# Kernel tuning notes

Hardware: AMD Instinct MI355X
Metric: run time of the kernel (lower is better)

Reference implementation:

```python
import jax, jax.numpy as jnp
import numpy as np

N_NODES = 131072
N_EDGES = 262144
N_GRAPHS = 4096
EMB = 300
N_LAYERS = 5
N_TASKS = 12
N_EXPERTS = 8
GATE_DIM = 300
NUM_ATOM_TYPE = 120
NUM_CHIRALITY = 3
NUM_BOND_TYPE = 6
NUM_BOND_DIR = 3


def setup_inputs() -> dict:
    key = jax.random.key(0)
    ks = jax.random.split(key, 24)
    x = jnp.stack([
        jax.random.randint(ks[0], (N_NODES,), 0, NUM_ATOM_TYPE),
        jax.random.randint(ks[1], (N_NODES,), 0, NUM_CHIRALITY),
    ], axis=1)
    edge_index = jax.random.randint(ks[2], (2, N_EDGES), 0, N_NODES)
    edge_attr = jnp.stack([
        jax.random.randint(ks[3], (N_EDGES,), 0, NUM_BOND_TYPE),
        jax.random.randint(ks[4], (N_EDGES,), 0, NUM_BOND_DIR),
    ], axis=1)
    batch = jnp.sort(jax.random.randint(ks[5], (N_NODES,), 0, N_GRAPHS))

    s = 0.05
    atom_emb1 = jax.random.normal(ks[6], (NUM_ATOM_TYPE, EMB)) * s
    atom_emb2 = jax.random.normal(ks[7], (NUM_CHIRALITY, EMB)) * s
    edge_emb1 = jax.random.normal(ks[8], (N_LAYERS, NUM_BOND_TYPE, EMB)) * s
    edge_emb2 = jax.random.normal(ks[9], (N_LAYERS, NUM_BOND_DIR, EMB)) * s
    mlp_w1 = jax.random.normal(ks[10], (N_LAYERS, EMB, 2 * EMB)) * s
    mlp_b1 = jnp.zeros((N_LAYERS, 2 * EMB))
    mlp_w2 = jax.random.normal(ks[11], (N_LAYERS, 2 * EMB, EMB)) * s
    mlp_b2 = jnp.zeros((N_LAYERS, EMB))
    bn_gamma = jnp.ones((N_LAYERS, EMB))
    bn_beta = jnp.zeros((N_LAYERS, EMB))
    gate_w1 = jax.random.normal(ks[12], (EMB, GATE_DIM)) * s
    gate_b1 = jnp.zeros((GATE_DIM,))
    gate_bn_g = jnp.ones((GATE_DIM,))
    gate_bn_b = jnp.zeros((GATE_DIM,))
    gate_w2 = jax.random.normal(ks[13], (GATE_DIM, GATE_DIM)) * s
    gate_b2 = jnp.zeros((GATE_DIM,))
    cluster = jax.random.normal(ks[14], (N_EXPERTS, GATE_DIM)) * s
    experts_w = jax.random.normal(ks[15], (EMB, N_TASKS * N_EXPERTS)) * s
    experts_b = jnp.zeros((N_TASKS * N_EXPERTS,))
    return dict(x=x, edge_index=edge_index, edge_attr=edge_attr, batch=batch,
                atom_emb1=atom_emb1, atom_emb2=atom_emb2,
                edge_emb1=edge_emb1, edge_emb2=edge_emb2,
                mlp_w1=mlp_w1, mlp_b1=mlp_b1, mlp_w2=mlp_w2, mlp_b2=mlp_b2,
                bn_gamma=bn_gamma, bn_beta=bn_beta,
                gate_w1=gate_w1, gate_b1=gate_b1,
                gate_bn_g=gate_bn_g, gate_bn_b=gate_bn_b,
                gate_w2=gate_w2, gate_b2=gate_b2,
                cluster=cluster, experts_w=experts_w, experts_b=experts_b)


def _batchnorm(h, g, b, eps=1e-5):
    mu = h.mean(axis=0)
    var = h.var(axis=0)
    return g * (h - mu) * jax.lax.rsqrt(var + eps) + b


def _forward(x, edge_index, edge_attr, batch,
             atom_emb1, atom_emb2, edge_emb1, edge_emb2,
             mlp_w1, mlp_b1, mlp_w2, mlp_b2, bn_gamma, bn_beta,
             gate_w1, gate_b1, gate_bn_g, gate_bn_b, gate_w2, gate_b2,
             cluster, experts_w, experts_b):
    n = x.shape[0]
    src, dst = edge_index[0], edge_index[1]
    ea0, ea1 = edge_attr[:, 0], edge_attr[:, 1]
    # node input embedding
    h = atom_emb1[x[:, 0]] + atom_emb2[x[:, 1]]  # [N, EMB]
    n_layers = mlp_w1.shape[0]
    for l in range(n_layers):
        ee = edge_emb1[l][ea0] + edge_emb2[l][ea1]  # [E, EMB]
        # self loops: attr = (bond_type=4, dir=0) for every node
        self_ee = edge_emb1[l][4] + edge_emb2[l][0]  # [EMB]
        agg = jax.ops.segment_sum(h[src] + ee, dst, num_segments=n)
        agg = agg + h + self_ee  # self-loop messages
        hid = jax.nn.relu(agg @ mlp_w1[l] + mlp_b1[l])
        h = hid @ mlp_w2[l] + mlp_b2[l]
        h = _batchnorm(h, bn_gamma[l], bn_beta[l])
        if l < n_layers - 1:
            h = jax.nn.relu(h)
    # graph pooling (JK='last')
    sums = jax.ops.segment_sum(h, batch, num_segments=N_GRAPHS)  # [B, EMB]
    counts = jax.ops.segment_sum(jnp.ones((n, 1), h.dtype), batch, num_segments=N_GRAPHS)
    gnn_out = sums / jnp.maximum(counts, 1.0)  # mean pool
    gate_input = sums  # global_add_pool
    # experts head: sum(gnn_out[:, :, None] * W, dim=1) + b == gnn_out @ W + b
    n_experts = cluster.shape[0]
    clf_logit = (gnn_out @ experts_w + experts_b).reshape(N_GRAPHS, -1, n_experts)
    # gate network
    zh = _batchnorm(gate_input @ gate_w1 + gate_b1, gate_bn_g, gate_bn_b)
    z = jax.nn.relu(zh) @ gate_w2 + gate_b2  # [B, GATE_DIM]
    # q: temperature-scaled softmax over cosine similarity to cluster centroids
    zn = z / jnp.maximum(jnp.linalg.norm(z, axis=1, keepdims=True), 1e-6)
    cn = cluster / jnp.maximum(jnp.linalg.norm(cluster, axis=1, keepdims=True), 1e-6)
    q = jax.nn.softmax(10.0 * (zn @ cn.T), axis=-1)  # T = 10
    return clf_logit, z, q


def reference(x, edge_index, edge_attr, batch,
              atom_emb1, atom_emb2, edge_emb1, edge_emb2,
              mlp_w1, mlp_b1, mlp_w2, mlp_b2, bn_gamma, bn_beta,
              gate_w1, gate_b1, gate_bn_g, gate_bn_b, gate_w2, gate_b2,
              cluster, experts_w, experts_b):
    return _forward(x, edge_index, edge_attr, batch,
                    atom_emb1, atom_emb2, edge_emb1, edge_emb2,
                    mlp_w1, mlp_b1, mlp_w2, mlp_b2, bn_gamma, bn_beta,
                    gate_w1, gate_b1, gate_bn_g, gate_bn_b, gate_w2, gate_b2,
                    cluster, experts_w, experts_b)
```

## Files before the change

kernel.cpp:

```cpp
#include <hip/hip_runtime.h>
#include <hip/hip_bf16.h>

typedef unsigned short u16;
typedef unsigned int u32;

#define NN 131072
#define NE 262144
#define NG 4096
#define EMB 300
#define HID 600
#define NL 5
#define NTNE 96
#define NEXP 8

#define W1T_ROWS 640
#define W1T_K    328
#define W2T_ROWS 384
#define W2T_K    648

typedef __attribute__((ext_vector_type(8)))  short  s16x8;
typedef __attribute__((ext_vector_type(8)))  __bf16 b16x8;
typedef __attribute__((ext_vector_type(16))) float  f32x16;

static __device__ __forceinline__ float u2f(u16 u) {
    union { u32 i; float f; } w; w.i = ((u32)u) << 16; return w.f;
}
static __device__ __forceinline__ u16 f2u(float f) {
    union { float f; u32 i; } w; w.f = f;
    return (u16)((w.i + 0x7fffu + ((w.i >> 16) & 1u)) >> 16);
}

static __device__ __forceinline__ f32x16 mfma_3216(s16x8 a, s16x8 b, f32x16 c) {
    return __builtin_amdgcn_mfma_f32_32x32x16_bf16(
        __builtin_bit_cast(b16x8, a), __builtin_bit_cast(b16x8, b), c, 0, 0, 0);
}

__global__ void k_zero(float* __restrict__ p, int n) {
    int i = blockIdx.x * 256 + threadIdx.x;
    if (i < n) p[i] = 0.f;
}
__global__ void k_zero_int(int* __restrict__ p, int n) {
    int i = blockIdx.x * 256 + threadIdx.x;
    if (i < n) p[i] = 0;
}

__global__ void k_embed(const int* __restrict__ x, const float* __restrict__ ae1,
                        const float* __restrict__ ae2, u16* __restrict__ h) {
    int i = blockIdx.x;
    int a0 = x[2 * i], a1 = x[2 * i + 1];
    for (int f = threadIdx.x; f < EMB; f += blockDim.x)
        h[(size_t)i * EMB + f] = f2u(ae1[a0 * EMB + f] + ae2[a1 * EMB + f]);
}

__global__ void k_hist(const int* __restrict__ ei, int* __restrict__ deg) {
    int e = blockIdx.x * 256 + threadIdx.x;
    if (e < NE) atomicAdd(&deg[ei[NE + e]], 1);
}

__global__ __launch_bounds__(1024) void k_scan(const int* __restrict__ deg,
                                               int* __restrict__ rowstart) {
    __shared__ int lds[1024];
    int tid = threadIdx.x;
    int base = tid * 128;
    int s = 0;
    for (int j = 0; j < 128; ++j) s += deg[base + j];
    lds[tid] = s;
    __syncthreads();
    for (int off = 1; off < 1024; off <<= 1) {
        int v = (tid >= off) ? lds[tid - off] : 0;
        __syncthreads();
        lds[tid] += v;
        __syncthreads();
    }
    int run = (tid == 0) ? 0 : lds[tid - 1];
    for (int j = 0; j < 128; ++j) {
        rowstart[base + j] = run;
        run += deg[base + j];
    }
    if (tid == 1023) rowstart[NN] = run;
}

__global__ void k_fill(const int* __restrict__ ei, const int* __restrict__ ea,
                       int* __restrict__ deg, const int* __restrict__ rowstart,
                       u32* __restrict__ payload) {
    int e = blockIdx.x * 256 + threadIdx.x;
    if (e >= NE) return;
    int src = ei[e], dst = ei[NE + e];
    int c = ea[2 * e] * 3 + ea[2 * e + 1];
    int old = atomicSub(&deg[dst], 1);
    int pos = rowstart[dst] + old - 1;
    payload[pos] = (u32)src | ((u32)c << 17);
}

__global__ void k_prep_w1(const float* __restrict__ w1, u16* __restrict__ w1t) {
    int n = blockIdx.x;
    int l = blockIdx.y;
    size_t dst = ((size_t)l * W1T_ROWS + n) * W1T_K;
    for (int k = threadIdx.x; k < W1T_K; k += blockDim.x) {
        u16 v = 0;
        if (n < HID && k < EMB) v = f2u(w1[(size_t)l * EMB * HID + (size_t)k * HID + n]);
        w1t[dst + k] = v;
    }
}
__global__ void k_prep_w2(const float* __restrict__ w2, u16* __restrict__ w2t) {
    int n = blockIdx.x;
    int l = blockIdx.y;
    size_t dst = ((size_t)l * W2T_ROWS + n) * W2T_K;
    for (int k = threadIdx.x; k < W2T_K; k += blockDim.x) {
        u16 v = 0;
        if (n < EMB && k < HID) v = f2u(w2[(size_t)l * HID * EMB + (size_t)k * EMB + n]);
        w2t[dst + k] = v;
    }
}

template <bool APPLY_BN>
__global__ __launch_bounds__(512) void k_layer1(const u16* __restrict__ h,
                                                const u32* __restrict__ payload,
                                                const int* __restrict__ rowstart,
                                                const float* __restrict__ e1,
                                                const float* __restrict__ e2,
                                                const float* __restrict__ stats,
                                                const float* __restrict__ bg,
                                                const float* __restrict__ bb,
                                                float invM,
                                                const u16* __restrict__ w1t,
                                                const float* __restrict__ b1,
                                                u16* __restrict__ hid) {
    __shared__ __align__(16) u16 ee_lds[18 * 300];
    __shared__ __align__(16) u16 scale_s[300];
    __shared__ __align__(16) u16 shift_s[300];
    __shared__ __align__(16) u16 A_s[64 * 328];
    int tid = threadIdx.x;
    int lane = tid & 63, wid = tid >> 6;
    int wr = wid >> 2, wc = wid & 3;
    int l31 = lane & 31, lhi = lane >> 5;
    size_t rowBase = (size_t)blockIdx.x * 64;

    for (int idx = tid; idx < 18 * 300; idx += 512) {
        int c = idx / 300, f = idx - c * 300;
        ee_lds[idx] = f2u(e1[(c / 3) * 300 + f] + e2[(c % 3) * 300 + f]);
    }
    if (APPLY_BN) {
        if (tid < 300) {
            float mu = stats[tid] * invM;
            float var = stats[EMB + tid] * invM - mu * mu;
            float sc = bg[tid] * rsqrtf(var + 1e-5f);
            scale_s[tid] = f2u(sc);
            shift_s[tid] = f2u(bb[tid] - mu * sc);
        }
    }
    for (int idx = tid; idx < 64 * 28; idx += 512)
        A_s[(idx / 28) * 328 + 300 + (idx % 28)] = 0;
    __syncthreads();

    for (int task = tid; task < 64 * 75; task += 512) {
        int r = task / 75, fc = task - r * 75;
        int i = (int)rowBase + r;
        int f0 = fc * 4;
        int beg = rowstart[i], end = rowstart[i + 1];
        float sc0 = 1.f, sc1 = 1.f, sc2 = 1.f, sc3 = 1.f;
        float sh0 = 0.f, sh1 = 0.f, sh2 = 0.f, sh3 = 0.f;
        if (APPLY_BN) {
            ushort4 scv = *(const ushort4*)&scale_s[f0];
            ushort4 shv = *(const ushort4*)&shift_s[f0];
            sc0 = u2f(scv.x); sc1 = u2f(scv.y); sc2 = u2f(scv.z); sc3 = u2f(scv.w);
            sh0 = u2f(shv.x); sh1 = u2f(shv.y); sh2 = u2f(shv.z); sh3 = u2f(shv.w);
        }
        ushort4 hv = *(const ushort4*)&h[(size_t)i * EMB + f0];
        ushort4 ev = *(const ushort4*)&ee_lds[12 * 300 + f0];
        float a0 = u2f(hv.x), a1 = u2f(hv.y), a2 = u2f(hv.z), a3 = u2f(hv.w);
        if (APPLY_BN) {
            a0 = fmaxf(a0 * sc0 + sh0, 0.f);
            a1 = fmaxf(a1 * sc1 + sh1, 0.f);
            a2 = fmaxf(a2 * sc2 + sh2, 0.f);
            a3 = fmaxf(a3 * sc3 + sh3, 0.f);
        }
        float v0 = a0 + u2f(ev.x), v1 = a1 + u2f(ev.y);
        float v2 = a2 + u2f(ev.z), v3 = a3 + u2f(ev.w);
        for (int e = beg; e < end; ++e) {
            u32 p = payload[e];
            int src = p & 0x1FFFF;
            ushort4 ec = *(const ushort4*)&ee_lds[(int)(p >> 17) * 300 + f0];
            ushort4 sv = *(const ushort4*)&h[(size_t)src * EMB + f0];
            float g0 = u2f(sv.x), g1 = u2f(sv.y), g2 = u2f(sv.z), g3 = u2f(sv.w);
            if (APPLY_BN) {
                g0 = fmaxf(g0 * sc0 + sh0, 0.f);
                g1 = fmaxf(g1 * sc1 + sh1, 0.f);
                g2 = fmaxf(g2 * sc2 + sh2, 0.f);
                g3 = fmaxf(g3 * sc3 + sh3, 0.f);
            }
            v0 += g0 + u2f(ec.x);
            v1 += g1 + u2f(ec.y);
            v2 += g2 + u2f(ec.z);
            v3 += g3 + u2f(ec.w);
        }
        short4 o;
        o.x = (short)f2u(v0); o.y = (short)f2u(v1);
        o.z = (short)f2u(v2); o.w = (short)f2u(v3);
        *(short4*)&A_s[r * 328 + f0] = o;
    }
    __syncthreads();

    s16x8 afr[20];
    int abase = (wr * 32 + l31) * 328 + lhi * 8;
#pragma unroll
    for (int s = 0; s < 20; ++s) afr[s] = *(const s16x8*)&A_s[abase + s * 16];

    for (int c5 = 0; c5 < 5; ++c5) {
        int col = c5 * 128 + wc * 32 + l31;
        const u16* bp = w1t + (size_t)col * W1T_K + lhi * 8;
        f32x16 acc = {};
#pragma unroll
        for (int s = 0; s < 20; ++s)
            acc = mfma_3216(afr[s], *(const s16x8*)&bp[s * 16], acc);
        if (col < HID) {
            float bias = b1[col];
#pragma unroll
            for (int r = 0; r < 16; ++r) {
                int row = (r & 3) + 8 * (r >> 2) + 4 * lhi;
                hid[(rowBase + wr * 32 + row) * HID + col] =
                    f2u(fmaxf(acc[r] + bias, 0.f));
            }
        }
    }
}

__global__ __launch_bounds__(256) void k_gemm2(const u16* __restrict__ hid,
                                               const u16* __restrict__ w2t,
                                               const float* __restrict__ b2,
                                               u16* __restrict__ hout) {
    __shared__ __align__(16) u16 A_s[64 * 72];
    __shared__ __align__(16) u16 B_s[128 * 72];
    int tid = threadIdx.x;
    int lane = tid & 63, wid = tid >> 6;
    int wr = wid >> 1, wc = wid & 1;
    int l31 = lane & 31, lhi = lane >> 5;
    size_t rowBase = (size_t)blockIdx.x * 64;
    int cc = blockIdx.y * 128;

    f32x16 acc0 = {}, acc1 = {};
    int aoff = (wr * 32 + l31) * 72 + lhi * 8;
    int boff0 = (wc * 64 + l31) * 72 + lhi * 8;
    int boff1 = boff0 + 32 * 72;

    for (int sl = 0; sl < 10; ++sl) {
        int k0 = sl * 64;
        for (int idx = tid; idx < 512; idx += 256) {
            int m = idx >> 3, kv = idx & 7;
            int k = k0 + kv * 8;
            s16x8 v = {};
            if (k < HID) v = *(const s16x8*)&hid[(rowBase + m) * HID + k];
            *(s16x8*)&A_s[m * 72 + kv * 8] = v;
        }
        for (int idx = tid; idx < 1024; idx += 256) {
            int n = idx >> 3, kv = idx & 7;
            *(s16x8*)&B_s[n * 72 + kv * 8] =
                *(const s16x8*)&w2t[(size_t)(cc + n) * W2T_K + k0 + kv * 8];
        }
        __syncthreads();

        int smax = (sl < 9) ? 4 : 2;
        for (int s = 0; s < smax; ++s) {
            s16x8 a  = *(const s16x8*)&A_s[aoff + s * 16];
            s16x8 ba = *(const s16x8*)&B_s[boff0 + s * 16];
            s16x8 bb = *(const s16x8*)&B_s[boff1 + s * 16];
            acc0 = mfma_3216(a, ba, acc0);
            acc1 = mfma_3216(a, bb, acc1);
        }
        __syncthreads();
    }

    int colA = cc + wc * 64 + l31;
    int colB = colA + 32;
    if (colA < EMB) {
        float bias = b2[colA];
#pragma unroll
        for (int r = 0; r < 16; ++r) {
            int row = (r & 3) + 8 * (r >> 2) + 4 * lhi;
            hout[(rowBase + wr * 32 + row) * EMB + colA] = f2u(acc0[r] + bias);
        }
    }
    if (colB < EMB) {
        float bias = b2[colB];
#pragma unroll
        for (int r = 0; r < 16; ++r) {
            int row = (r & 3) + 8 * (r >> 2) + 4 * lhi;
            hout[(rowBase + wr * 32 + row) * EMB + colB] = f2u(acc1[r] + bias);
        }
    }
}

__global__ void k_bn_stats_h(const u16* __restrict__ X, float* __restrict__ stats) {
    int t = threadIdx.x;
    int half = t / 160;
    int pr = t - half * 160;
    if (pr >= 150) return;
    float s0 = 0.f, s1 = 0.f, q0 = 0.f, q1 = 0.f;
    for (int r = blockIdx.x * 2 + half; r < NN; r += 512) {
        u32 v = *(const u32*)&X[(size_t)r * EMB + pr * 2];
        float a = u2f((u16)(v & 0xffff));
        float b = u2f((u16)(v >> 16));
        s0 += a; s1 += b; q0 += a * a; q1 += b * b;
    }
    atomicAdd(&stats[2 * pr], s0);
    atomicAdd(&stats[2 * pr + 1], s1);
    atomicAdd(&stats[EMB + 2 * pr], q0);
    atomicAdd(&stats[EMB + 2 * pr + 1], q1);
}

template <bool RELU>
__global__ void k_bn_apply_h(u16* __restrict__ X, const float* __restrict__ stats,
                             const float* __restrict__ g, const float* __restrict__ b, float invM) {
    int r = blockIdx.x;
    for (int f = threadIdx.x; f < EMB; f += blockDim.x) {
        float mu = stats[f] * invM;
        float var = stats[EMB + f] * invM - mu * mu;
        float v = (u2f(X[(size_t)r * EMB + f]) - mu) * rsqrtf(var + 1e-5f) * g[f] + b[f];
        if (RELU) v = fmaxf(v, 0.f);
        X[(size_t)r * EMB + f] = f2u(v);
    }
}

__global__ void k_bn_stats_f(const float* __restrict__ X, int M, float* __restrict__ stats) {
    int f = threadIdx.x;
    if (f >= EMB) return;
    float s = 0.f, s2 = 0.f;
    for (int r = blockIdx.x; r < M; r += gridDim.x) {
        float v = X[(size_t)r * EMB + f];
        s += v;
        s2 += v * v;
    }
    atomicAdd(&stats[f], s);
    atomicAdd(&stats[EMB + f], s2);
}

template <bool RELU>
__global__ void k_bn_apply_f(float* __restrict__ X, const float* __restrict__ stats,
                             const float* __restrict__ g, const float* __restrict__ b, float invM) {
    int r = blockIdx.x;
    for (int f = threadIdx.x; f < EMB; f += blockDim.x) {
// ... 124 lines not shown
        float v = z[(size_t)gi * EMB + f];
        s += v * v;
    }
    for (int o = 32; o; o >>= 1) s += __shfl_xor(s, o);
    float zn = fmaxf(sqrtf(s), 1e-6f);
    float sc[NEXP];
#pragma unroll
    for (int e = 0; e < NEXP; ++e) {
        float d = 0.f;
        for (int f = l; f < EMB; f += 64) d += z[(size_t)gi * EMB + f] * cluster[e * EMB + f];
        for (int o = 32; o; o >>= 1) d += __shfl_xor(d, o);
        sc[e] = 10.f * d / (zn * fmaxf(cnorm[e], 1e-6f));
    }
    float mx = sc[0];
#pragma unroll
    for (int e = 1; e < NEXP; ++e) mx = fmaxf(mx, sc[e]);
    float se = 0.f;
#pragma unroll
    for (int e = 0; e < NEXP; ++e) {
        sc[e] = expf(sc[e] - mx);
        se += sc[e];
    }
    if (l < NEXP) qout[(size_t)gi * NEXP + l] = sc[l] / se;
}

extern "C" void kernel_launch(void* const* d_in, const int* in_sizes, int n_in,
                              void* d_out, int out_size, void* d_ws, size_t ws_size,
                              hipStream_t stream) {
    const int* x       = (const int*)d_in[0];
    const int* ei      = (const int*)d_in[1];
    const int* ea      = (const int*)d_in[2];
    const int* batch   = (const int*)d_in[3];
    const float* ae1   = (const float*)d_in[4];
    const float* ae2   = (const float*)d_in[5];
    const float* ee1   = (const float*)d_in[6];
    const float* ee2   = (const float*)d_in[7];
    const float* w1    = (const float*)d_in[8];
    const float* b1    = (const float*)d_in[9];
    const float* w2    = (const float*)d_in[10];
    const float* b2    = (const float*)d_in[11];
    const float* bng   = (const float*)d_in[12];
    const float* bnb   = (const float*)d_in[13];
    const float* gw1   = (const float*)d_in[14];
    const float* gb1   = (const float*)d_in[15];
    const float* gbng  = (const float*)d_in[16];
    const float* gbnb  = (const float*)d_in[17];
    const float* gw2   = (const float*)d_in[18];
    const float* gb2   = (const float*)d_in[19];
    const float* clus  = (const float*)d_in[20];
    const float* ew    = (const float*)d_in[21];
    const float* eb    = (const float*)d_in[22];

    char* wp = (char*)d_ws;
    u16* hbuf = (u16*)wp;                 wp += (size_t)NN * EMB * sizeof(u16);
    u16* hid = (u16*)wp;                  wp += (size_t)NN * HID * sizeof(u16);
    float* stats = (float*)wp;            wp += 2 * EMB * sizeof(float);
    u16* w1t = (u16*)wp;                  wp += (size_t)NL * W1T_ROWS * W1T_K * sizeof(u16);
    u16* w2t = (u16*)wp;                  wp += (size_t)NL * W2T_ROWS * W2T_K * sizeof(u16);
    int* deg = (int*)wp;                  wp += (size_t)NN * sizeof(int);
    int* rowstart = (int*)wp;             wp += (size_t)(NN + 4) * sizeof(int);
    u32* payload = (u32*)wp;              wp += (size_t)NE * sizeof(u32);

    float* sums   = (float*)hid;
    float* counts = sums + (size_t)NG * EMB;
    float* zh     = counts + NG;
    float* zb     = zh + (size_t)NG * EMB;
    float* cnorm  = zb + (size_t)NG * EMB;

    float* out     = (float*)d_out;
    float* out_clf = out;
    float* out_z   = out + (size_t)NG * NTNE;
    float* out_q   = out_z + (size_t)NG * EMB;

    k_zero_int<<<NN / 256, 256, 0, stream>>>(deg, NN);
    k_hist<<<NE / 256, 256, 0, stream>>>(ei, deg);
    k_scan<<<1, 1024, 0, stream>>>(deg, rowstart);
    k_fill<<<NE / 256, 256, 0, stream>>>(ei, ea, deg, rowstart, payload);

    k_prep_w1<<<dim3(W1T_ROWS, NL), 64, 0, stream>>>(w1, w1t);
    k_prep_w2<<<dim3(W2T_ROWS, NL), 64, 0, stream>>>(w2, w2t);
    k_embed<<<NN, 320, 0, stream>>>(x, ae1, ae2, hbuf);

    for (int l = 0; l < NL; ++l) {
        const float* e1 = ee1 + (size_t)l * 6 * EMB;
        const float* e2 = ee2 + (size_t)l * 3 * EMB;
        if (l == 0)
            k_layer1<false><<<NN / 64, 512, 0, stream>>>(
                hbuf, payload, rowstart, e1, e2, nullptr, nullptr, nullptr, 0.f,
                w1t + (size_t)l * W1T_ROWS * W1T_K, b1 + (size_t)l * HID, hid);
        else
            k_layer1<true><<<NN / 64, 512, 0, stream>>>(
                hbuf, payload, rowstart, e1, e2, stats,
                bng + (size_t)(l - 1) * EMB, bnb + (size_t)(l - 1) * EMB, 1.f / NN,
                w1t + (size_t)l * W1T_ROWS * W1T_K, b1 + (size_t)l * HID, hid);
        k_gemm2<<<dim3(NN / 64, 3), 256, 0, stream>>>(hid, w2t + (size_t)l * W2T_ROWS * W2T_K,
                                                      b2 + (size_t)l * EMB, hbuf);
        k_zero<<<3, 256, 0, stream>>>(stats, 2 * EMB);
        k_bn_stats_h<<<256, 320, 0, stream>>>(hbuf, stats);
    }

    k_bn_apply_h<false><<<NN, 320, 0, stream>>>(hbuf, stats, bng + (size_t)(NL - 1) * EMB,
                                                bnb + (size_t)(NL - 1) * EMB, 1.f / NN);

    k_pool<<<NG, 320, 0, stream>>>(hbuf, batch, sums, counts);
    k_clf<<<NG, 128, 0, stream>>>(sums, counts, ew, eb, out_clf);

    k_gemm<false><<<dim3(5, NG / 64), 256, 0, stream>>>(sums, gw1, gb1, zh, NG, EMB, EMB);
    k_zero<<<3, 256, 0, stream>>>(stats, 2 * EMB);
    k_bn_stats_f<<<256, 320, 0, stream>>>(zh, NG, stats);
    k_bn_apply_f<true><<<NG, 320, 0, stream>>>(zh, stats, gbng, gbnb, 1.f / NG);
    k_gemm<false><<<dim3(5, NG / 64), 256, 0, stream>>>(zh, gw2, gb2, zb, NG, EMB, EMB);

    k_cnorm<<<1, 64, 0, stream>>>(clus, cnorm);
    k_zout<<<NG, 320, 0, stream>>>(zb, out_z);
    k_q<<<NG, 64, 0, stream>>>(zb, clus, cnorm, out_q);
}
```

Before: 3.047 ms.

## Fuse second MLP GEMM into layer kernel, keep hidden tile in LDS

The second GEMM is now computed inside the aggregation plus first-GEMM kernel. Each 128-column chunk of the hidden activation is staged in LDS and multiplied straight into three accumulators per wave, so the NN×600 bf16 hidden tensor is no longer written to and re-read from global memory. Because a block now reads neighbour rows of h while other blocks write the layer output, h is ping-ponged between two buffers. The edge gather loop is also unrolled by two to issue more loads per iteration. In exchange, w2 is read directly from global memory by every block, two extra block barriers are added per chunk, and LDS use grows by about 17 KB per block.

```diff
diff --git a/kernel.cpp b/kernel.cpp
--- a/kernel.cpp
+++ b/kernel.cpp
@@ -114,22 +114,25 @@
 }
 
 template <bool APPLY_BN>
-__global__ __launch_bounds__(512) void k_layer1(const u16* __restrict__ h,
-                                                const u32* __restrict__ payload,
-                                                const int* __restrict__ rowstart,
-                                                const float* __restrict__ e1,
-                                                const float* __restrict__ e2,
-                                                const float* __restrict__ stats,
-                                                const float* __restrict__ bg,
-                                                const float* __restrict__ bb,
-                                                float invM,
-                                                const u16* __restrict__ w1t,
-                                                const float* __restrict__ b1,
-                                                u16* __restrict__ hid) {
+__global__ __launch_bounds__(512, 4) void k_layer_fused(const u16* __restrict__ h,
+                                                        const u32* __restrict__ payload,
+                                                        const int* __restrict__ rowstart,
+                                                        const float* __restrict__ e1,
+                                                        const float* __restrict__ e2,
+                                                        const float* __restrict__ stats,
+                                                        const float* __restrict__ bg,
+                                                        const float* __restrict__ bb,
+                                                        float invM,
+                                                        const u16* __restrict__ w1t,
+                                                        const float* __restrict__ b1,
+                                                        const u16* __restrict__ w2t,
+                                                        const float* __restrict__ b2,
+                                                        u16* __restrict__ hout) {
     __shared__ __align__(16) u16 ee_lds[18 * 300];
     __shared__ __align__(16) u16 scale_s[300];
     __shared__ __align__(16) u16 shift_s[300];
     __shared__ __align__(16) u16 A_s[64 * 328];
+    __shared__ __align__(16) u16 H_s[64 * 136];
     int tid = threadIdx.x;
     int lane = tid & 63, wid = tid >> 6;
     int wr = wid >> 2, wc = wid & 3;
@@ -177,7 +180,28 @@
         }
         float v0 = a0 + u2f(ev.x), v1 = a1 + u2f(ev.y);
         float v2 = a2 + u2f(ev.z), v3 = a3 + u2f(ev.w);
-        for (int e = beg; e < end; ++e) {
+        int e = beg;
+        for (; e + 2 <= end; e += 2) {
+            u32 p0 = payload[e], p1 = payload[e + 1];
+            int sA = p0 & 0x1FFFF, sB = p1 & 0x1FFFF;
+            ushort4 svA = *(const ushort4*)&h[(size_t)sA * EMB + f0];
+            ushort4 svB = *(const ushort4*)&h[(size_t)sB * EMB + f0];
+            ushort4 ecA = *(const ushort4*)&ee_lds[(int)(p0 >> 17) * 300 + f0];
+            ushort4 ecB = *(const ushort4*)&ee_lds[(int)(p1 >> 17) * 300 + f0];
+            float gA0 = u2f(svA.x), gA1 = u2f(svA.y), gA2 = u2f(svA.z), gA3 = u2f(svA.w);
+            float gB0 = u2f(svB.x), gB1 = u2f(svB.y), gB2 = u2f(svB.z), gB3 = u2f(svB.w);
+            if (APPLY_BN) {
+                gA0 = fmaxf(gA0 * sc0 + sh0, 0.f); gB0 = fmaxf(gB0 * sc0 + sh0, 0.f);
+                gA1 = fmaxf(gA1 * sc1 + sh1, 0.f); gB1 = fmaxf(gB1 * sc1 + sh1, 0.f);
+                gA2 = fmaxf(gA2 * sc2 + sh2, 0.f); gB2 = fmaxf(gB2 * sc2 + sh2, 0.f);
+                gA3 = fmaxf(gA3 * sc3 + sh3, 0.f); gB3 = fmaxf(gB3 * sc3 + sh3, 0.f);
+            }
+            v0 += gA0 + u2f(ecA.x) + gB0 + u2f(ecB.x);
+            v1 += gA1 + u2f(ecA.y) + gB1 + u2f(ecB.y);
+            v2 += gA2 + u2f(ecA.z) + gB2 + u2f(ecB.z);
+            v3 += gA3 + u2f(ecA.w) + gB3 + u2f(ecB.w);
+        }
+        if (e < end) {
             u32 p = payload[e];
             int src = p & 0x1FFFF;
             ushort4 ec = *(const ushort4*)&ee_lds[(int)(p >> 17) * 300 + f0];
@@ -201,91 +225,72 @@
     }
     __syncthreads();
 
-    s16x8 afr[20];
+    f32x16 acc20 = {}, acc21 = {}, acc22 = {};
     int abase = (wr * 32 + l31) * 328 + lhi * 8;
-#pragma unroll
-    for (int s = 0; s < 20; ++s) afr[s] = *(const s16x8*)&A_s[abase + s * 16];
+    int arow2 = (wr * 32 + l31) * 136 + lhi * 8;
+    int colp = wc * 32 + l31;
 
     for (int c5 = 0; c5 < 5; ++c5) {
-        int col = c5 * 128 + wc * 32 + l31;
-        const u16* bp = w1t + (size_t)col * W1T_K + lhi * 8;
-        f32x16 acc = {};
+        int col1 = c5 * 128 + colp;
+        const u16* bp = w1t + (size_t)col1 * W1T_K + lhi * 8;
+        f32x16 acc1 = {};
 #pragma unroll
         for (int s = 0; s < 20; ++s)
-            acc = mfma_3216(afr[s], *(const s16x8*)&bp[s * 16], acc);
-        if (col < HID) {
-            float bias = b1[col];
+            acc1 = mfma_3216(*(const s16x8*)&A_s[abase + s * 16],
+                             *(const s16x8*)&bp[s * 16], acc1);
+        bool valid = col1 < HID;
+        float bias1 = valid ? b1[col1] : 0.f;
+#pragma unroll
+        for (int r = 0; r < 16; ++r) {
+            int row = (r & 3) + 8 * (r >> 2) + 4 * lhi;
+            float v = valid ? fmaxf(acc1[r] + bias1, 0.f) : 0.f;
+            H_s[(wr * 32 + row) * 136 + colp] = f2u(v);
+        }
+        __syncthreads();
+
+#pragma unroll
+        for (int kk = 0; kk < 8; ++kk) {
+            s16x8 a = *(const s16x8*)&H_s[arow2 + kk * 16];
+            int gk = c5 * 128 + kk * 16 + lhi * 8;
+            const u16* wb = w2t + gk;
+            acc20 = mfma_3216(a, *(const s16x8*)&wb[(size_t)(wc * 96 + l31) * W2T_K], acc20);
+            acc21 = mfma_3216(a, *(const s16x8*)&wb[(size_t)(wc * 96 + 32 + l31) * W2T_K], acc21);
+            acc22 = mfma_3216(a, *(const s16x8*)&wb[(size_t)(wc * 96 + 64 + l31) * W2T_K], acc22);
+        }
+        __syncthreads();
+    }
+
+    {
+        int col = wc * 96 + l31;
+        if (col < EMB) {
+            float bias = b2[col];
 #pragma unroll
             for (int r = 0; r < 16; ++r) {
                 int row = (r & 3) + 8 * (r >> 2) + 4 * lhi;
-                hid[(rowBase + wr * 32 + row) * HID + col] =
-                    f2u(fmaxf(acc[r] + bias, 0.f));
+                hout[(rowBase + wr * 32 + row) * EMB + col] = f2u(acc20[r] + bias);
             }
         }
     }
-}
-
-__global__ __launch_bounds__(256) void k_gemm2(const u16* __restrict__ hid,
-                                               const u16* __restrict__ w2t,
-                                               const float* __restrict__ b2,
-                                               u16* __restrict__ hout) {
-    __shared__ __align__(16) u16 A_s[64 * 72];
-    __shared__ __align__(16) u16 B_s[128 * 72];
-    int tid = threadIdx.x;
-    int lane = tid & 63, wid = tid >> 6;
-    int wr = wid >> 1, wc = wid & 1;
-    int l31 = lane & 31, lhi = lane >> 5;
-    size_t rowBase = (size_t)blockIdx.x * 64;
-    int cc = blockIdx.y * 128;
-
-    f32x16 acc0 = {}, acc1 = {};
-    int aoff = (wr * 32 + l31) * 72 + lhi * 8;
-    int boff0 = (wc * 64 + l31) * 72 + lhi * 8;
-    int boff1 = boff0 + 32 * 72;
-
-    for (int sl = 0; sl < 10; ++sl) {
-        int k0 = sl * 64;
-        for (int idx = tid; idx < 512; idx += 256) {
-            int m = idx >> 3, kv = idx & 7;
-            int k = k0 + kv * 8;
-            s16x8 v = {};
-            if (k < HID) v = *(const s16x8*)&hid[(rowBase + m) * HID + k];
-            *(s16x8*)&A_s[m * 72 + kv * 8] = v;
-        }
-        for (int idx = tid; idx < 1024; idx += 256) {
-            int n = idx >> 3, kv = idx & 7;
-            *(s16x8*)&B_s[n * 72 + kv * 8] =
-                *(const s16x8*)&w2t[(size_t)(cc + n) * W2T_K + k0 + kv * 8];
-        }
-        __syncthreads();
-
-        int smax = (sl < 9) ? 4 : 2;
-        for (int s = 0; s < smax; ++s) {
-            s16x8 a  = *(const s16x8*)&A_s[aoff + s * 16];
-            s16x8 ba = *(const s16x8*)&B_s[boff0 + s * 16];
-            s16x8 bb = *(const s16x8*)&B_s[boff1 + s * 16];
-            acc0 = mfma_3216(a, ba, acc0);
-            acc1 = mfma_3216(a, bb, acc1);
-        }
-        __syncthreads();
-    }
-
-    int colA = cc + wc * 64 + l31;
-    int colB = colA + 32;
-    if (colA < EMB) {
-        float bias = b2[colA];
-#pragma unroll
-        for (int r = 0; r < 16; ++r) {
-            int row = (r & 3) + 8 * (r >> 2) + 4 * lhi;
-            hout[(rowBase + wr * 32 + row) * EMB + colA] = f2u(acc0[r] + bias);
-        }
-    }
-    if (colB < EMB) {
-        float bias = b2[colB];
-#pragma unroll
-        for (int r = 0; r < 16; ++r) {
-            int row = (r & 3) + 8 * (r >> 2) + 4 * lhi;
-            hout[(rowBase + wr * 32 + row) * EMB + colB] = f2u(acc1[r] + bias);
+    {
+        int col = wc * 96 + 32 + l31;
+        if (col < EMB) {
+            float bias = b2[col];
+#pragma unroll
+            for (int r = 0; r < 16; ++r) {
+                int row = (r & 3) + 8 * (r >> 2) + 4 * lhi;
+                hout[(rowBase + wr * 32 + row) * EMB + col] = f2u(acc21[r] + bias);
+            }
+        }
+    }
+    {
+        int col = wc * 96 + 64 + l31;
+        if (col < EMB) {
+            float bias = b2[col];
+#pragma unroll
+            for (int r = 0; r < 16; ++r) {
+                int row = (r & 3) + 8 * (r >> 2) + 4 * lhi;
+                hout[(rowBase + wr * 32 + row) * EMB + col] = f2u(acc22[r] + bias);
+            }
         }
     }
 }
@@ -516,8 +521,9 @@
     const float* eb    = (const float*)d_in[22];
 
     char* wp = (char*)d_ws;
-    u16* hbuf = (u16*)wp;                 wp += (size_t)NN * EMB * sizeof(u16);
-    u16* hid = (u16*)wp;                  wp += (size_t)NN * HID * sizeof(u16);
+    u16* hA = (u16*)wp;                   wp += (size_t)NN * EMB * sizeof(u16);
+    u16* hB = (u16*)wp;                   wp += (size_t)NN * EMB * sizeof(u16);
+    float* scratch = (float*)wp;          wp += ((size_t)NG * EMB * 3 + NG + NEXP + 64) * sizeof(float);
     float* stats = (float*)wp;            wp += 2 * EMB * sizeof(float);
     u16* w1t = (u16*)wp;                  wp += (size_t)NL * W1T_ROWS * W1T_K * sizeof(u16);
     u16* w2t = (u16*)wp;                  wp += (size_t)NL * W2T_ROWS * W2T_K * sizeof(u16);
@@ -525,7 +531,7 @@
     int* rowstart = (int*)wp;             wp += (size_t)(NN + 4) * sizeof(int);
     u32* payload = (u32*)wp;              wp += (size_t)NE * sizeof(u32);
 
-    float* sums   = (float*)hid;
+    float* sums   = scratch;
     float* counts = sums + (size_t)NG * EMB;
     float* zh     = counts + NG;
     float* zb     = zh + (size_t)NG * EMB;
@@ -543,30 +549,33 @@
 
     k_prep_w1<<<dim3(W1T_ROWS, NL), 64, 0, stream>>>(w1, w1t);
     k_prep_w2<<<dim3(W2T_ROWS, NL), 64, 0, stream>>>(w2, w2t);
-    k_embed<<<NN, 320, 0, stream>>>(x, ae1, ae2, hbuf);
-
+    k_embed<<<NN, 320, 0, stream>>>(x, ae1, ae2, hA);
+
+    u16* hin = hA;
+    u16* hno = hB;
     for (int l = 0; l < NL; ++l) {
         const float* e1 = ee1 + (size_t)l * 6 * EMB;
         const float* e2 = ee2 + (size_t)l * 3 * EMB;
         if (l == 0)
-            k_layer1<false><<<NN / 64, 512, 0, stream>>>(
-                hbuf, payload, rowstart, e1, e2, nullptr, nullptr, nullptr, 0.f,
-                w1t + (size_t)l * W1T_ROWS * W1T_K, b1 + (size_t)l * HID, hid);
+            k_layer_fused<false><<<NN / 64, 512, 0, stream>>>(
+                hin, payload, rowstart, e1, e2, nullptr, nullptr, nullptr, 0.f,
+                w1t + (size_t)l * W1T_ROWS * W1T_K, b1 + (size_t)l * HID,
+                w2t + (size_t)l * W2T_ROWS * W2T_K, b2 + (size_t)l * EMB, hno);
         else
-            k_layer1<true><<<NN / 64, 512, 0, stream>>>(
-                hbuf, payload, rowstart, e1, e2, stats,
+            k_layer_fused<true><<<NN / 64, 512, 0, stream>>>(
+                hin, payload, rowstart, e1, e2, stats,
                 bng + (size_t)(l - 1) * EMB, bnb + (size_t)(l - 1) * EMB, 1.f / NN,
-                w1t + (size_t)l * W1T_ROWS * W1T_K, b1 + (size_t)l * HID, hid);
-        k_gemm2<<<dim3(NN / 64, 3), 256, 0, stream>>>(hid, w2t + (size_t)l * W2T_ROWS * W2T_K,
-                                                      b2 + (size_t)l * EMB, hbuf);
+                w1t + (size_t)l * W1T_ROWS * W1T_K, b1 + (size_t)l * HID,
+                w2t + (size_t)l * W2T_ROWS * W2T_K, b2 + (size_t)l * EMB, hno);
         k_zero<<<3, 256, 0, stream>>>(stats, 2 * EMB);
-        k_bn_stats_h<<<256, 320, 0, stream>>>(hbuf, stats);
-    }
-
-    k_bn_apply_h<false><<<NN, 320, 0, stream>>>(hbuf, stats, bng + (size_t)(NL - 1) * EMB,
+        k_bn_stats_h<<<256, 320, 0, stream>>>(hno, stats);
+        u16* t = hin; hin = hno; hno = t;
+    }
+
+    k_bn_apply_h<false><<<NN, 320, 0, stream>>>(hin, stats, bng + (size_t)(NL - 1) * EMB,
                                                 bnb + (size_t)(NL - 1) * EMB, 1.f / NN);
 
-    k_pool<<<NG, 320, 0, stream>>>(hbuf, batch, sums, counts);
+    k_pool<<<NG, 320, 0, stream>>>(hin, batch, sums, counts);
     k_clf<<<NG, 128, 0, stream>>>(sums, counts, ew, eb, out_clf);
 
     k_gemm<false><<<dim3(5, NG / 64), 256, 0, stream>>>(sums, gw1, gb1, zh, NG, EMB, EMB);
```

Result: slower. 3.221 ms (+5.7%).

## Precompute edge embeddings and BN params globally; gather two rows per thread

Applied to the files above, without the earlier changes.

Moves the per-block construction of the 18 combined edge-embedding rows and the BN scale/shift into small one-time prep kernels that write bf16 tables to global memory. The aggregation loop then reads those tables through the cache instead of LDS, which cuts per-block setup work and LDS use. Each thread now handles two destination rows at once, interleaving their neighbour gathers to expose more memory-level parallelism. The cost is extra global and cache traffic for the edge-table lookups, higher register pressure, and two small extra launches.

```diff
diff --git a/kernel.cpp b/kernel.cpp
--- a/kernel.cpp
+++ b/kernel.cpp
@@ -17,6 +17,7 @@
 #define W1T_K    328
 #define W2T_ROWS 384
 #define W2T_K    648
+#define EE_S     304
 
 typedef __attribute__((ext_vector_type(8)))  short  s16x8;
 typedef __attribute__((ext_vector_type(8)))  __bf16 b16x8;
@@ -113,22 +114,43 @@
     }
 }
 
+__global__ void k_prep_ee(const float* __restrict__ ee1, const float* __restrict__ ee2,
+                          u16* __restrict__ eeT) {
+    int c = blockIdx.x;
+    int l = blockIdx.y;
+    size_t dst = ((size_t)l * 18 + c) * EE_S;
+    const float* e1 = ee1 + (size_t)l * 6 * EMB + (c / 3) * EMB;
+    const float* e2 = ee2 + (size_t)l * 3 * EMB + (c % 3) * EMB;
+    for (int f = threadIdx.x; f < EE_S; f += blockDim.x)
+        eeT[dst + f] = (f < EMB) ? f2u(e1[f] + e2[f]) : (u16)0;
+}
+
+__global__ void k_prep_bn(const float* __restrict__ stats, const float* __restrict__ bg,
+                          const float* __restrict__ bb, float invM,
+                          u16* __restrict__ scT, u16* __restrict__ shT) {
+    int t = threadIdx.x;
+    if (t >= EE_S) return;
+    if (t < EMB) {
+        float mu = stats[t] * invM;
+        float var = stats[EMB + t] * invM - mu * mu;
+        float sc = bg[t] * rsqrtf(var + 1e-5f);
+        scT[t] = f2u(sc);
+        shT[t] = f2u(bb[t] - mu * sc);
+    } else {
+        scT[t] = 0; shT[t] = 0;
+    }
+}
+
 template <bool APPLY_BN>
 __global__ __launch_bounds__(512) void k_layer1(const u16* __restrict__ h,
                                                 const u32* __restrict__ payload,
                                                 const int* __restrict__ rowstart,
-                                                const float* __restrict__ e1,
-                                                const float* __restrict__ e2,
-                                                const float* __restrict__ stats,
-                                                const float* __restrict__ bg,
-                                                const float* __restrict__ bb,
-                                                float invM,
+                                                const u16* __restrict__ eeT,
+                                                const u16* __restrict__ scT,
+                                                const u16* __restrict__ shT,
                                                 const u16* __restrict__ w1t,
                                                 const float* __restrict__ b1,
                                                 u16* __restrict__ hid) {
-    __shared__ __align__(16) u16 ee_lds[18 * 300];
-    __shared__ __align__(16) u16 scale_s[300];
-    __shared__ __align__(16) u16 shift_s[300];
     __shared__ __align__(16) u16 A_s[64 * 328];
     int tid = threadIdx.x;
     int lane = tid & 63, wid = tid >> 6;
@@ -136,52 +158,68 @@
     int l31 = lane & 31, lhi = lane >> 5;
     size_t rowBase = (size_t)blockIdx.x * 64;
 
-    for (int idx = tid; idx < 18 * 300; idx += 512) {
-        int c = idx / 300, f = idx - c * 300;
-        ee_lds[idx] = f2u(e1[(c / 3) * 300 + f] + e2[(c % 3) * 300 + f]);
-    }
-    if (APPLY_BN) {
-        if (tid < 300) {
-            float mu = stats[tid] * invM;
-            float var = stats[EMB + tid] * invM - mu * mu;
-            float sc = bg[tid] * rsqrtf(var + 1e-5f);
-            scale_s[tid] = f2u(sc);
-            shift_s[tid] = f2u(bb[tid] - mu * sc);
-        }
-    }
     for (int idx = tid; idx < 64 * 28; idx += 512)
         A_s[(idx / 28) * 328 + 300 + (idx % 28)] = 0;
     __syncthreads();
 
-    for (int task = tid; task < 64 * 75; task += 512) {
-        int r = task / 75, fc = task - r * 75;
-        int i = (int)rowBase + r;
+    for (int task = tid; task < 32 * 75; task += 512) {
+        int pr = task / 75, fc = task - pr * 75;
         int f0 = fc * 4;
-        int beg = rowstart[i], end = rowstart[i + 1];
+        int iA = (int)rowBase + pr;
+        int iB = iA + 32;
+        int begA = rowstart[iA], endA = rowstart[iA + 1];
+        int begB = rowstart[iB], endB = rowstart[iB + 1];
         float sc0 = 1.f, sc1 = 1.f, sc2 = 1.f, sc3 = 1.f;
         float sh0 = 0.f, sh1 = 0.f, sh2 = 0.f, sh3 = 0.f;
         if (APPLY_BN) {
-            ushort4 scv = *(const ushort4*)&scale_s[f0];
-            ushort4 shv = *(const ushort4*)&shift_s[f0];
+            ushort4 scv = *(const ushort4*)&scT[f0];
+            ushort4 shv = *(const ushort4*)&shT[f0];
             sc0 = u2f(scv.x); sc1 = u2f(scv.y); sc2 = u2f(scv.z); sc3 = u2f(scv.w);
             sh0 = u2f(shv.x); sh1 = u2f(shv.y); sh2 = u2f(shv.z); sh3 = u2f(shv.w);
         }
-        ushort4 hv = *(const ushort4*)&h[(size_t)i * EMB + f0];
-        ushort4 ev = *(const ushort4*)&ee_lds[12 * 300 + f0];
-        float a0 = u2f(hv.x), a1 = u2f(hv.y), a2 = u2f(hv.z), a3 = u2f(hv.w);
+        ushort4 ev = *(const ushort4*)&eeT[12 * EE_S + f0];
+        float e0 = u2f(ev.x), e1v = u2f(ev.y), e2v = u2f(ev.z), e3 = u2f(ev.w);
+
+        ushort4 hvA = *(const ushort4*)&h[(size_t)iA * EMB + f0];
+        ushort4 hvB = *(const ushort4*)&h[(size_t)iB * EMB + f0];
+        float vA0 = u2f(hvA.x), vA1 = u2f(hvA.y), vA2 = u2f(hvA.z), vA3 = u2f(hvA.w);
+        float vB0 = u2f(hvB.x), vB1 = u2f(hvB.y), vB2 = u2f(hvB.z), vB3 = u2f(hvB.w);
         if (APPLY_BN) {
-            a0 = fmaxf(a0 * sc0 + sh0, 0.f);
-            a1 = fmaxf(a1 * sc1 + sh1, 0.f);
-            a2 = fmaxf(a2 * sc2 + sh2, 0.f);
-            a3 = fmaxf(a3 * sc3 + sh3, 0.f);
-        }
-        float v0 = a0 + u2f(ev.x), v1 = a1 + u2f(ev.y);
-        float v2 = a2 + u2f(ev.z), v3 = a3 + u2f(ev.w);
-        for (int e = beg; e < end; ++e) {
-            u32 p = payload[e];
+            vA0 = fmaxf(vA0 * sc0 + sh0, 0.f); vB0 = fmaxf(vB0 * sc0 + sh0, 0.f);
+            vA1 = fmaxf(vA1 * sc1 + sh1, 0.f); vB1 = fmaxf(vB1 * sc1 + sh1, 0.f);
+            vA2 = fmaxf(vA2 * sc2 + sh2, 0.f); vB2 = fmaxf(vB2 * sc2 + sh2, 0.f);
+            vA3 = fmaxf(vA3 * sc3 + sh3, 0.f); vB3 = fmaxf(vB3 * sc3 + sh3, 0.f);
+        }
+        vA0 += e0; vA1 += e1v; vA2 += e2v; vA3 += e3;
+        vB0 += e0; vB1 += e1v; vB2 += e2v; vB3 += e3;
+
+        int eA = begA, eB = begB;
+        while (eA < endA && eB < endB) {
+            u32 pA = payload[eA], pB = payload[eB];
+            int sA = pA & 0x1FFFF, sB = pB & 0x1FFFF;
+            ushort4 svA = *(const ushort4*)&h[(size_t)sA * EMB + f0];
+            ushort4 svB = *(const ushort4*)&h[(size_t)sB * EMB + f0];
+            ushort4 ecA = *(const ushort4*)&eeT[(size_t)(pA >> 17) * EE_S + f0];
+            ushort4 ecB = *(const ushort4*)&eeT[(size_t)(pB >> 17) * EE_S + f0];
+            float gA0 = u2f(svA.x), gA1 = u2f(svA.y), gA2 = u2f(svA.z), gA3 = u2f(svA.w);
+            float gB0 = u2f(svB.x), gB1 = u2f(svB.y), gB2 = u2f(svB.z), gB3 = u2f(svB.w);
+            if (APPLY_BN) {
+                gA0 = fmaxf(gA0 * sc0 + sh0, 0.f); gB0 = fmaxf(gB0 * sc0 + sh0, 0.f);
+                gA1 = fmaxf(gA1 * sc1 + sh1, 0.f); gB1 = fmaxf(gB1 * sc1 + sh1, 0.f);
+                gA2 = fmaxf(gA2 * sc2 + sh2, 0.f); gB2 = fmaxf(gB2 * sc2 + sh2, 0.f);
+                gA3 = fmaxf(gA3 * sc3 + sh3, 0.f); gB3 = fmaxf(gB3 * sc3 + sh3, 0.f);
+            }
+            vA0 += gA0 + u2f(ecA.x); vB0 += gB0 + u2f(ecB.x);
+            vA1 += gA1 + u2f(ecA.y); vB1 += gB1 + u2f(ecB.y);
+            vA2 += gA2 + u2f(ecA.z); vB2 += gB2 + u2f(ecB.z);
+            vA3 += gA3 + u2f(ecA.w); vB3 += gB3 + u2f(ecB.w);
+            ++eA; ++eB;
+        }
+        for (; eA < endA; ++eA) {
+            u32 p = payload[eA];
             int src = p & 0x1FFFF;
-            ushort4 ec = *(const ushort4*)&ee_lds[(int)(p >> 17) * 300 + f0];
             ushort4 sv = *(const ushort4*)&h[(size_t)src * EMB + f0];
+            ushort4 ec = *(const ushort4*)&eeT[(size_t)(p >> 17) * EE_S + f0];
             float g0 = u2f(sv.x), g1 = u2f(sv.y), g2 = u2f(sv.z), g3 = u2f(sv.w);
             if (APPLY_BN) {
                 g0 = fmaxf(g0 * sc0 + sh0, 0.f);
@@ -189,15 +227,35 @@
                 g2 = fmaxf(g2 * sc2 + sh2, 0.f);
                 g3 = fmaxf(g3 * sc3 + sh3, 0.f);
             }
-            v0 += g0 + u2f(ec.x);
-            v1 += g1 + u2f(ec.y);
-            v2 += g2 + u2f(ec.z);
-            v3 += g3 + u2f(ec.w);
-        }
-        short4 o;
-        o.x = (short)f2u(v0); o.y = (short)f2u(v1);
-        o.z = (short)f2u(v2); o.w = (short)f2u(v3);
-        *(short4*)&A_s[r * 328 + f0] = o;
+            vA0 += g0 + u2f(ec.x);
+            vA1 += g1 + u2f(ec.y);
+            vA2 += g2 + u2f(ec.z);
+            vA3 += g3 + u2f(ec.w);
+        }
+        for (; eB < endB; ++eB) {
+            u32 p = payload[eB];
+            int src = p & 0x1FFFF;
+            ushort4 sv = *(const ushort4*)&h[(size_t)src * EMB + f0];
+            ushort4 ec = *(const ushort4*)&eeT[(size_t)(p >> 17) * EE_S + f0];
+            float g0 = u2f(sv.x), g1 = u2f(sv.y), g2 = u2f(sv.z), g3 = u2f(sv.w);
+            if (APPLY_BN) {
+                g0 = fmaxf(g0 * sc0 + sh0, 0.f);
+                g1 = fmaxf(g1 * sc1 + sh1, 0.f);
+                g2 = fmaxf(g2 * sc2 + sh2, 0.f);
+                g3 = fmaxf(g3 * sc3 + sh3, 0.f);
+            }
+            vB0 += g0 + u2f(ec.x);
+            vB1 += g1 + u2f(ec.y);
+            vB2 += g2 + u2f(ec.z);
+            vB3 += g3 + u2f(ec.w);
+        }
+        short4 oA, oB;
+        oA.x = (short)f2u(vA0); oA.y = (short)f2u(vA1);
+        oA.z = (short)f2u(vA2); oA.w = (short)f2u(vA3);
+        oB.x = (short)f2u(vB0); oB.y = (short)f2u(vB1);
+        oB.z = (short)f2u(vB2); oB.w = (short)f2u(vB3);
+        *(short4*)&A_s[pr * 328 + f0] = oA;
+        *(short4*)&A_s[(pr + 32) * 328 + f0] = oB;
     }
     __syncthreads();
 
@@ -521,6 +579,9 @@
     float* stats = (float*)wp;            wp += 2 * EMB * sizeof(float);
     u16* w1t = (u16*)wp;                  wp += (size_t)NL * W1T_ROWS * W1T_K * sizeof(u16);
     u16* w2t = (u16*)wp;                  wp += (size_t)NL * W2T_ROWS * W2T_K * sizeof(u16);
+    u16* eeT = (u16*)wp;                  wp += (size_t)NL * 18 * EE_S * sizeof(u16);
+    u16* scT = (u16*)wp;                  wp += EE_S * sizeof(u16);
+    u16* shT = (u16*)wp;                  wp += EE_S * sizeof(u16);
     int* deg = (int*)wp;                  wp += (size_t)NN * sizeof(int);
     int* rowstart = (int*)wp;             wp += (size_t)(NN + 4) * sizeof(int);
     u32* payload = (u32*)wp;              wp += (size_t)NE * sizeof(u32);
@@ -543,24 +604,26 @@
 
     k_prep_w1<<<dim3(W1T_ROWS, NL), 64, 0, stream>>>(w1, w1t);
     k_prep_w2<<<dim3(W2T_ROWS, NL), 64, 0, stream>>>(w2, w2t);
+    k_prep_ee<<<dim3(18, NL), 128, 0, stream>>>(ee1, ee2, eeT);
     k_embed<<<NN, 320, 0, stream>>>(x, ae1, ae2, hbuf);
 
     for (int l = 0; l < NL; ++l) {
-        const float* e1 = ee1 + (size_t)l * 6 * EMB;
-        const float* e2 = ee2 + (size_t)l * 3 * EMB;
+        const u16* eeL = eeT + (size_t)l * 18 * EE_S;
         if (l == 0)
             k_layer1<false><<<NN / 64, 512, 0, stream>>>(
-                hbuf, payload, rowstart, e1, e2, nullptr, nullptr, nullptr, 0.f,
+                hbuf, payload, rowstart, eeL, nullptr, nullptr,
                 w1t + (size_t)l * W1T_ROWS * W1T_K, b1 + (size_t)l * HID, hid);
         else
             k_layer1<true><<<NN / 64, 512, 0, stream>>>(
-                hbuf, payload, rowstart, e1, e2, stats,
-                bng + (size_t)(l - 1) * EMB, bnb + (size_t)(l - 1) * EMB, 1.f / NN,
+                hbuf, payload, rowstart, eeL, scT, shT,
                 w1t + (size_t)l * W1T_ROWS * W1T_K, b1 + (size_t)l * HID, hid);
         k_gemm2<<<dim3(NN / 64, 3), 256, 0, stream>>>(hid, w2t + (size_t)l * W2T_ROWS * W2T_K,
                                                       b2 + (size_t)l * EMB, hbuf);
         k_zero<<<3, 256, 0, stream>>>(stats, 2 * EMB);
         k_bn_stats_h<<<256, 320, 0, stream>>>(hbuf, stats);
+        if (l < NL - 1)
+            k_prep_bn<<<1, 320, 0, stream>>>(stats, bng + (size_t)l * EMB,
+                                             bnb + (size_t)l * EMB, 1.f / NN, scT, shT);
     }
 
     k_bn_apply_h<false><<<NN, 320, 0, stream>>>(hbuf, stats, bng + (size_t)(NL - 1) * EMB,
```

Result: no change. 3.006 ms, median of 3 (-1.3%).

## Precompute edge embeddings and BN affine once; shrink layer1 blocks to 32 rows

Applied to the files above, without the earlier changes.

Edge-embedding sums and the BatchNorm scale/shift are now computed once by small prep kernels instead of in every layer1 block's shared memory. That lets layer1 use 32-row, 256-thread blocks with much less LDS, which should raise occupancy and hide gather latency. The gemm2 grid is also transposed so the three column tiles of a row block run adjacently, improving L2 reuse of the A rows. In exchange, edge-embedding lookups become global/L1 reads rather than LDS reads, and each W1 tile is reloaded by twice as many blocks.

```diff
diff --git a/kernel.cpp b/kernel.cpp
--- a/kernel.cpp
+++ b/kernel.cpp
@@ -17,6 +17,7 @@
 #define W1T_K    328
 #define W2T_ROWS 384
 #define W2T_K    648
+#define EE_S     304
 
 typedef __attribute__((ext_vector_type(8)))  short  s16x8;
 typedef __attribute__((ext_vector_type(8)))  __bf16 b16x8;
@@ -113,61 +114,68 @@
     }
 }
 
+__global__ void k_prep_ee(const float* __restrict__ ee1, const float* __restrict__ ee2,
+                          u16* __restrict__ eeT) {
+    int c = blockIdx.x;
+    int l = blockIdx.y;
+    size_t dst = ((size_t)l * 18 + c) * EE_S;
+    const float* e1 = ee1 + (size_t)l * 6 * EMB + (c / 3) * EMB;
+    const float* e2 = ee2 + (size_t)l * 3 * EMB + (c % 3) * EMB;
+    for (int f = threadIdx.x; f < EE_S; f += blockDim.x)
+        eeT[dst + f] = (f < EMB) ? f2u(e1[f] + e2[f]) : (u16)0;
+}
+
+__global__ void k_prep_bn(const float* __restrict__ stats, const float* __restrict__ bg,
+                          const float* __restrict__ bb, float invM,
+                          u16* __restrict__ scT, u16* __restrict__ shT) {
+    int t = threadIdx.x;
+    if (t >= EE_S) return;
+    if (t < EMB) {
+        float mu = stats[t] * invM;
+        float var = stats[EMB + t] * invM - mu * mu;
+        float sc = bg[t] * rsqrtf(var + 1e-5f);
+        scT[t] = f2u(sc);
+        shT[t] = f2u(bb[t] - mu * sc);
+    } else {
+        scT[t] = 0; shT[t] = 0;
+    }
+}
+
 template <bool APPLY_BN>
-__global__ __launch_bounds__(512) void k_layer1(const u16* __restrict__ h,
+__global__ __launch_bounds__(256) void k_layer1(const u16* __restrict__ h,
                                                 const u32* __restrict__ payload,
                                                 const int* __restrict__ rowstart,
-                                                const float* __restrict__ e1,
-                                                const float* __restrict__ e2,
-                                                const float* __restrict__ stats,
-                                                const float* __restrict__ bg,
-                                                const float* __restrict__ bb,
-                                                float invM,
+                                                const u16* __restrict__ eeT,
+                                                const u16* __restrict__ scT,
+                                                const u16* __restrict__ shT,
                                                 const u16* __restrict__ w1t,
                                                 const float* __restrict__ b1,
                                                 u16* __restrict__ hid) {
-    __shared__ __align__(16) u16 ee_lds[18 * 300];
-    __shared__ __align__(16) u16 scale_s[300];
-    __shared__ __align__(16) u16 shift_s[300];
-    __shared__ __align__(16) u16 A_s[64 * 328];
+    __shared__ __align__(16) u16 A_s[32 * 328];
     int tid = threadIdx.x;
-    int lane = tid & 63, wid = tid >> 6;
-    int wr = wid >> 2, wc = wid & 3;
+    int lane = tid & 63, wc = tid >> 6;
     int l31 = lane & 31, lhi = lane >> 5;
-    size_t rowBase = (size_t)blockIdx.x * 64;
-
-    for (int idx = tid; idx < 18 * 300; idx += 512) {
-        int c = idx / 300, f = idx - c * 300;
-        ee_lds[idx] = f2u(e1[(c / 3) * 300 + f] + e2[(c % 3) * 300 + f]);
-    }
-    if (APPLY_BN) {
-        if (tid < 300) {
-            float mu = stats[tid] * invM;
-            float var = stats[EMB + tid] * invM - mu * mu;
-            float sc = bg[tid] * rsqrtf(var + 1e-5f);
-            scale_s[tid] = f2u(sc);
-            shift_s[tid] = f2u(bb[tid] - mu * sc);
-        }
-    }
-    for (int idx = tid; idx < 64 * 28; idx += 512)
+    size_t rowBase = (size_t)blockIdx.x * 32;
+
+    for (int idx = tid; idx < 32 * 28; idx += 256)
         A_s[(idx / 28) * 328 + 300 + (idx % 28)] = 0;
     __syncthreads();
 
-    for (int task = tid; task < 64 * 75; task += 512) {
+    for (int task = tid; task < 32 * 75; task += 256) {
         int r = task / 75, fc = task - r * 75;
+        int f0 = fc * 4;
         int i = (int)rowBase + r;
-        int f0 = fc * 4;
         int beg = rowstart[i], end = rowstart[i + 1];
         float sc0 = 1.f, sc1 = 1.f, sc2 = 1.f, sc3 = 1.f;
         float sh0 = 0.f, sh1 = 0.f, sh2 = 0.f, sh3 = 0.f;
         if (APPLY_BN) {
-            ushort4 scv = *(const ushort4*)&scale_s[f0];
-            ushort4 shv = *(const ushort4*)&shift_s[f0];
+            ushort4 scv = *(const ushort4*)&scT[f0];
+            ushort4 shv = *(const ushort4*)&shT[f0];
             sc0 = u2f(scv.x); sc1 = u2f(scv.y); sc2 = u2f(scv.z); sc3 = u2f(scv.w);
             sh0 = u2f(shv.x); sh1 = u2f(shv.y); sh2 = u2f(shv.z); sh3 = u2f(shv.w);
         }
         ushort4 hv = *(const ushort4*)&h[(size_t)i * EMB + f0];
-        ushort4 ev = *(const ushort4*)&ee_lds[12 * 300 + f0];
+        ushort4 ev = *(const ushort4*)&eeT[12 * EE_S + f0];
         float a0 = u2f(hv.x), a1 = u2f(hv.y), a2 = u2f(hv.z), a3 = u2f(hv.w);
         if (APPLY_BN) {
             a0 = fmaxf(a0 * sc0 + sh0, 0.f);
@@ -180,8 +188,8 @@
         for (int e = beg; e < end; ++e) {
             u32 p = payload[e];
             int src = p & 0x1FFFF;
-            ushort4 ec = *(const ushort4*)&ee_lds[(int)(p >> 17) * 300 + f0];
             ushort4 sv = *(const ushort4*)&h[(size_t)src * EMB + f0];
+            ushort4 ec = *(const ushort4*)&eeT[(size_t)(p >> 17) * EE_S + f0];
             float g0 = u2f(sv.x), g1 = u2f(sv.y), g2 = u2f(sv.z), g3 = u2f(sv.w);
             if (APPLY_BN) {
                 g0 = fmaxf(g0 * sc0 + sh0, 0.f);
@@ -202,7 +210,7 @@
     __syncthreads();
 
     s16x8 afr[20];
-    int abase = (wr * 32 + l31) * 328 + lhi * 8;
+    int abase = l31 * 328 + lhi * 8;
 #pragma unroll
     for (int s = 0; s < 20; ++s) afr[s] = *(const s16x8*)&A_s[abase + s * 16];
 
@@ -218,7 +226,7 @@
 #pragma unroll
             for (int r = 0; r < 16; ++r) {
                 int row = (r & 3) + 8 * (r >> 2) + 4 * lhi;
-                hid[(rowBase + wr * 32 + row) * HID + col] =
+                hid[(rowBase + row) * HID + col] =
                     f2u(fmaxf(acc[r] + bias, 0.f));
             }
         }
@@ -235,8 +243,8 @@
     int lane = tid & 63, wid = tid >> 6;
     int wr = wid >> 1, wc = wid & 1;
     int l31 = lane & 31, lhi = lane >> 5;
-    size_t rowBase = (size_t)blockIdx.x * 64;
-    int cc = blockIdx.y * 128;
+    size_t rowBase = (size_t)blockIdx.y * 64;
+    int cc = blockIdx.x * 128;
 
     f32x16 acc0 = {}, acc1 = {};
     int aoff = (wr * 32 + l31) * 72 + lhi * 8;
@@ -521,6 +529,9 @@
     float* stats = (float*)wp;            wp += 2 * EMB * sizeof(float);
     u16* w1t = (u16*)wp;                  wp += (size_t)NL * W1T_ROWS * W1T_K * sizeof(u16);
     u16* w2t = (u16*)wp;                  wp += (size_t)NL * W2T_ROWS * W2T_K * sizeof(u16);
+    u16* eeT = (u16*)wp;                  wp += (size_t)NL * 18 * EE_S * sizeof(u16);
+    u16* scT = (u16*)wp;                  wp += EE_S * sizeof(u16);
+    u16* shT = (u16*)wp;                  wp += EE_S * sizeof(u16);
     int* deg = (int*)wp;                  wp += (size_t)NN * sizeof(int);
     int* rowstart = (int*)wp;             wp += (size_t)(NN + 4) * sizeof(int);
     u32* payload = (u32*)wp;              wp += (size_t)NE * sizeof(u32);
@@ -543,24 +554,26 @@
 
     k_prep_w1<<<dim3(W1T_ROWS, NL), 64, 0, stream>>>(w1, w1t);
     k_prep_w2<<<dim3(W2T_ROWS, NL), 64, 0, stream>>>(w2, w2t);
+    k_prep_ee<<<dim3(18, NL), 128, 0, stream>>>(ee1, ee2, eeT);
     k_embed<<<NN, 320, 0, stream>>>(x, ae1, ae2, hbuf);
 
     for (int l = 0; l < NL; ++l) {
-        const float* e1 = ee1 + (size_t)l * 6 * EMB;
-        const float* e2 = ee2 + (size_t)l * 3 * EMB;
+        const u16* eeL = eeT + (size_t)l * 18 * EE_S;
         if (l == 0)
-            k_layer1<false><<<NN / 64, 512, 0, stream>>>(
-                hbuf, payload, rowstart, e1, e2, nullptr, nullptr, nullptr, 0.f,
+            k_layer1<false><<<NN / 32, 256, 0, stream>>>(
+                hbuf, payload, rowstart, eeL, nullptr, nullptr,
                 w1t + (size_t)l * W1T_ROWS * W1T_K, b1 + (size_t)l * HID, hid);
         else
-            k_layer1<true><<<NN / 64, 512, 0, stream>>>(
-                hbuf, payload, rowstart, e1, e2, stats,
-                bng + (size_t)(l - 1) * EMB, bnb + (size_t)(l - 1) * EMB, 1.f / NN,
+            k_layer1<true><<<NN / 32, 256, 0, stream>>>(
+                hbuf, payload, rowstart, eeL, scT, shT,
                 w1t + (size_t)l * W1T_ROWS * W1T_K, b1 + (size_t)l * HID, hid);
-        k_gemm2<<<dim3(NN / 64, 3), 256, 0, stream>>>(hid, w2t + (size_t)l * W2T_ROWS * W2T_K,
+        k_gemm2<<<dim3(3, NN / 64), 256, 0, stream>>>(hid, w2t + (size_t)l * W2T_ROWS * W2T_K,
                                                       b2 + (size_t)l * EMB, hbuf);
         k_zero<<<3, 256, 0, stream>>>(stats, 2 * EMB);
         k_bn_stats_h<<<256, 320, 0, stream>>>(hbuf, stats);
+        if (l < NL - 1)
+            k_prep_bn<<<1, 320, 0, stream>>>(stats, bng + (size_t)l * EMB,
+                                             bnb + (size_t)l * EMB, 1.f / NN, scT, shT);
     }
 
     k_bn_apply_h<false><<<NN, 320, 0, stream>>>(hbuf, stats, bng + (size_t)(NL - 1) * EMB,
```

Result: no change. 3.055 ms (+0.3%).
